# Kernel optimization log

Hardware: AMD Instinct MI355X
Metric: run time of the kernel (lower is better)

The kernel has to match this reference:

```python
import jax, jax.numpy as jnp
import numpy as np

D_MODEL = 1024
NUM_EXPERTS = 8
TOP_K = 2
B, S = 1, 2048


def setup_inputs() -> dict:
    key = jax.random.key(0)
    ks = jax.random.split(key, 8)
    sd = 1.0 / np.sqrt(D_MODEL)
    x = jax.random.normal(ks[0], (B, S, D_MODEL), dtype=jnp.float32)
    gate_w = jax.random.normal(ks[1], (D_MODEL, NUM_EXPERTS), dtype=jnp.float32) * sd
    gate_b = jnp.zeros((NUM_EXPERTS,), dtype=jnp.float32)
    w1 = jax.random.normal(ks[2], (NUM_EXPERTS, D_MODEL, 8 * D_MODEL), dtype=jnp.float32) * sd
    b1 = jnp.zeros((NUM_EXPERTS, 8 * D_MODEL), dtype=jnp.float32)
    w2 = jax.random.normal(ks[3], (NUM_EXPERTS, 4 * D_MODEL, D_MODEL), dtype=jnp.float32) * (1.0 / np.sqrt(4 * D_MODEL))
    b2 = jnp.zeros((NUM_EXPERTS, D_MODEL), dtype=jnp.float32)
    return {"x": x, "gate_w": gate_w, "gate_b": gate_b, "w1": w1, "b1": b1, "w2": w2, "b2": b2}


def reference(x, gate_w, gate_b, w1, b1, w2, b2):
    # Gating: top-k logits, softmax over the selected k
    gate_logits = jnp.einsum('bsd,de->bse', x, gate_w) + gate_b          # [B,S,E]
    weights, indices = jax.lax.top_k(gate_logits, TOP_K)                  # [B,S,K]
    weights = jax.nn.softmax(weights, axis=-1)

    # Dense all-expert compute (matches original masked-sum math; dropout in eval)
    h = jnp.einsum('bsd,edh->ebsh', x, w1) + b1[:, None, None, :]         # [E,B,S,8D]
    xh, gh = jnp.split(h, 2, axis=-1)                                     # each [E,B,S,4D]
    act = jax.nn.silu(gh) * xh
    out_e = jnp.einsum('ebsf,efd->ebsd', act, w2) + b2[:, None, None, :]  # [E,B,S,D]

    # Combine: gather the top-k expert outputs per token and weight-sum
    out_e = jnp.transpose(out_e, (1, 2, 0, 3))                            # [B,S,E,D]
    sel = jnp.take_along_axis(out_e, indices[..., None], axis=2)          # [B,S,K,D]
    return jnp.sum(sel * weights[..., None], axis=2)                      # [B,S,D]
```

## Files before the change

### kernel.cpp

```cpp
#include <hip/hip_runtime.h>
#include <hip/hip_bf16.h>

#define S 2048
#define D 1024
#define NE 8
#define HF 4096
#define HH 8192
#define BK 32
#define ACT_ROWS 4224
#define MAXRB 40
#define MAXRB2 24

typedef __attribute__((ext_vector_type(8))) __bf16 bf16x8;
typedef __attribute__((ext_vector_type(4))) float f32x4;

__device__ __forceinline__ unsigned cvtpk(float lo, float hi) {
  unsigned r;
  asm("v_cvt_pk_bf16_f32 %0, %1, %2" : "=v"(r) : "v"(lo), "v"(hi));
  return r;
}
__device__ __forceinline__ unsigned bf16b(float f) {
  unsigned b = __float_as_uint(f);
  return (b + 0x7fffu + ((b >> 16) & 1u)) >> 16;
}
__device__ __forceinline__ void gll16(const ushort* g, ushort* l) {
  __builtin_amdgcn_global_load_lds(
      (const __attribute__((address_space(1))) void*)g,
      (__attribute__((address_space(3))) void*)l, 16, 0, 0);
}

__global__ __launch_bounds__(256) void gate_kernel(
    const float* __restrict__ x, const float* __restrict__ gw,
    const float* __restrict__ gb, ushort* __restrict__ xb,
    int* __restrict__ mi0, int* __restrict__ mi1,
    float* __restrict__ mw0, float* __restrict__ mw1) {
  const int t = blockIdx.x;
  const int l = threadIdx.x;
  const float4 xv = ((const float4*)(x + (size_t)t * D))[l];
  uint2 wv = {cvtpk(xv.x, xv.y), cvtpk(xv.z, xv.w)};
  ((uint2*)(xb + (size_t)t * D))[l] = wv;

  float xa[4] = {xv.x, xv.y, xv.z, xv.w};
  float acc[NE];
#pragma unroll
  for (int e = 0; e < NE; ++e) acc[e] = 0.f;
  const float* g0 = gw + (size_t)(4 * l) * NE;
#pragma unroll
  for (int j = 0; j < 4; ++j)
#pragma unroll
    for (int e = 0; e < NE; ++e) acc[e] += xa[j] * g0[j * NE + e];
#pragma unroll
  for (int e = 0; e < NE; ++e) {
    float v = acc[e];
#pragma unroll
    for (int off = 32; off > 0; off >>= 1) v += __shfl_xor(v, off);
    acc[e] = v;
  }
  __shared__ float sm[4][NE];
  const int wid = l >> 6;
  if ((l & 63) == 0) {
#pragma unroll
    for (int e = 0; e < NE; ++e) sm[wid][e] = acc[e];
  }
  __syncthreads();
  if (l == 0) {
    float lg[NE];
#pragma unroll
    for (int e = 0; e < NE; ++e)
      lg[e] = sm[0][e] + sm[1][e] + sm[2][e] + sm[3][e] + gb[e];
    int i0 = 0; float m0 = lg[0];
#pragma unroll
    for (int e = 1; e < NE; ++e) if (lg[e] > m0) { m0 = lg[e]; i0 = e; }
    int i1 = -1; float m1 = -3.4e38f;
#pragma unroll
    for (int e = 0; e < NE; ++e) if (e != i0 && lg[e] > m1) { m1 = lg[e]; i1 = e; }
    float p = __expf(m1 - m0);
    float inv = 1.f / (1.f + p);
    mi0[t] = i0; mi1[t] = i1;
    mw0[t] = inv; mw1[t] = p * inv;
  }
}

__global__ __launch_bounds__(1024) void route_kernel(
    const int* __restrict__ mi0, const int* __restrict__ mi1,
    int* __restrict__ counts, int* __restrict__ basep, int* __restrict__ list_tok,
    int* __restrict__ mr0, int* __restrict__ mr1,
    int* __restrict__ rb_e, int* __restrict__ rb_row0, int* __restrict__ rb_n,
    int* __restrict__ rb2_e, int* __restrict__ rb2_row0, int* __restrict__ rb2_n) {
  __shared__ int cnt[NE];
  __shared__ int cur[NE];
  const int t = threadIdx.x;
  if (t < NE) cnt[t] = 0;
  __syncthreads();
  const int e0a = mi0[t], e1a = mi1[t];
  const int e0b = mi0[t + 1024], e1b = mi1[t + 1024];
  atomicAdd(&cnt[e0a], 1); atomicAdd(&cnt[e1a], 1);
  atomicAdd(&cnt[e0b], 1); atomicAdd(&cnt[e1b], 1);
  __syncthreads();
  if (t == 0) {
    int s = 0;
#pragma unroll
    for (int e = 0; e < NE; ++e) { basep[e] = s; cur[e] = s; s += cnt[e]; }
    basep[NE] = s;
    int nrb = 0, nrb2 = 0;
    for (int e = 0; e < NE; ++e) {
      for (int r0 = 0; r0 < cnt[e]; r0 += 128) {
        rb_e[nrb] = e; rb_row0[nrb] = r0; ++nrb;
      }
      for (int r0 = 0; r0 < cnt[e]; r0 += 256) {
        rb2_e[nrb2] = e; rb2_row0[nrb2] = r0; ++nrb2;
      }
    }
    *rb_n = nrb;
    *rb2_n = nrb2;
  }
  if (t < NE) counts[t] = cnt[t];
  __syncthreads();
  int r;
  r = atomicAdd(&cur[e0a], 1); list_tok[r] = t; mr0[t] = r;
  r = atomicAdd(&cur[e1a], 1); list_tok[r] = t; mr1[t] = r;
  r = atomicAdd(&cur[e0b], 1); list_tok[r] = t + 1024; mr0[t + 1024] = r;
  r = atomicAdd(&cur[e1b], 1); list_tok[r] = t + 1024; mr1[t + 1024] = r;
}

__global__ __launch_bounds__(512) void gemm1_kernel(
    const ushort* __restrict__ xb, const float* __restrict__ w1,
    const float* __restrict__ b1, const int* __restrict__ counts,
    const int* __restrict__ basep, const int* __restrict__ list_tok,
    const int* __restrict__ rb2_e, const int* __restrict__ rb2_row0,
    const int* __restrict__ rb2_n, ushort* __restrict__ act_buf) {
  const int rb = blockIdx.y;
  if (rb >= *rb2_n) return;
  const int e = rb2_e[rb];
  const int row0 = rb2_row0[rb];
  const int cnt = counts[e];
  const int jt = blockIdx.x * 64;
  const float* __restrict__ Wf = w1 + (size_t)e * D * HH;
  const int gbase = basep[e];

  __shared__ ushort As[2][256][BK];
  __shared__ unsigned Bs[2][32][68];

  const int tid = threadIdx.x;
  const int w = tid >> 6;
  const int i = tid & 63;

  const int rA0 = w * 32 + (i >> 2);
  const int rA1 = rA0 + 16;
  int s0 = row0 + rA0; if (s0 >= cnt) s0 = cnt - 1;
  int s1 = row0 + rA1; if (s1 >= cnt) s1 = cnt - 1;
  const ushort* pa0 = xb + (size_t)list_tok[gbase + s0] * D + (i & 3) * 8;
  const ushort* pa1 = xb + (size_t)list_tok[gbase + s1] * D + (i & 3) * 8;

  const int half = tid >> 8;
  const int kp = (tid >> 4) & 15;
  const int n4 = (tid & 15) * 4;
  const float* pB = Wf + (size_t)(2 * kp) * HH + jt + n4 + half * HF;

  const int wm = (w >> 1) * 64;
  const int wn = (w & 1) * 32;
  const int lr = i & 15;
  const int kg = i >> 4;

  f32x4 acc[2][4][2] = {};

  {
    float4 b0v = *(const float4*)(pB);
    float4 b1v = *(const float4*)(pB + HH);
    uint4 u = {cvtpk(b0v.x, b1v.x), cvtpk(b0v.y, b1v.y),
               cvtpk(b0v.z, b1v.z), cvtpk(b0v.w, b1v.w)};
    *(uint4*)&Bs[0][half * 16 + kp][n4] = u;
  }
  gll16(pa0, &As[0][w * 32][0]);
  gll16(pa1, &As[0][w * 32 + 16][0]);
  __syncthreads();

  int cur = 0;
#pragma unroll 1
  for (int it = 0; it < D / BK; ++it) {
    const bool pf = (it + 1 < D / BK);
    float4 b0v, b1v;
    if (pf) {
      const size_t koff = (size_t)(it + 1) * BK * HH;
      b0v = *(const float4*)(pB + koff);
      b1v = *(const float4*)(pB + koff + HH);
      const int ko = (it + 1) * BK;
      gll16(pa0 + ko, &As[cur ^ 1][w * 32][0]);
      gll16(pa1 + ko, &As[cur ^ 1][w * 32 + 16][0]);
    }
    bf16x8 af[4], bfr[2][2];
#pragma unroll
    for (int mi = 0; mi < 4; ++mi)
      af[mi] = *(const bf16x8*)&As[cur][wm + mi * 16 + lr][kg * 8];
#pragma unroll
    for (int h = 0; h < 2; ++h)
#pragma unroll
      for (int ni = 0; ni < 2; ++ni) {
        const int col = wn + ni * 16 + lr;
        uint4 tv;
        tv.x = Bs[cur][h * 16 + kg * 4 + 0][col];
        tv.y = Bs[cur][h * 16 + kg * 4 + 1][col];
        tv.z = Bs[cur][h * 16 + kg * 4 + 2][col];
        tv.w = Bs[cur][h * 16 + kg * 4 + 3][col];
        bfr[h][ni] = *(const bf16x8*)&tv;
      }
#pragma unroll
    for (int h = 0; h < 2; ++h)
#pragma unroll
      for (int mi = 0; mi < 4; ++mi)
#pragma unroll
        for (int ni = 0; ni < 2; ++ni)
          acc[h][mi][ni] = __builtin_amdgcn_mfma_f32_16x16x32_bf16(af[mi], bfr[h][ni],
                                                                   acc[h][mi][ni], 0, 0, 0);
    if (pf) {
      uint4 u = {cvtpk(b0v.x, b1v.x), cvtpk(b0v.y, b1v.y),
                 cvtpk(b0v.z, b1v.z), cvtpk(b0v.w, b1v.w)};
      *(uint4*)&Bs[cur ^ 1][half * 16 + kp][n4] = u;
    }
    __syncthreads();
    cur ^= 1;
  }

#pragma unroll
  for (int mi = 0; mi < 4; ++mi)
#pragma unroll
    for (int ni = 0; ni < 2; ++ni) {
      const int c = jt + wn + ni * 16 + lr;
      const float bx = b1[(size_t)e * HH + c];
      const float bg = b1[(size_t)e * HH + HF + c];
      f32x4 vx = acc[0][mi][ni];
      f32x4 vg = acc[1][mi][ni];
#pragma unroll
      for (int q = 0; q < 4; ++q) {
        const int slot = row0 + wm + mi * 16 + kg * 4 + q;
        if (slot < cnt) {
          float xv = vx[q] + bx;
          float g = vg[q] + bg;
          float a = g / (1.f + __expf(-g)) * xv;
          act_buf[(size_t)(gbase + slot) * HF + c] = (ushort)bf16b(a);
        }
      }
    }
}

__global__ __launch_bounds__(256) void gemm2_kernel(
    const ushort* __restrict__ act_buf, const float* __restrict__ w2,
    const int* __restrict__ counts, const int* __restrict__ basep,
    const int* __restrict__ rb_e, const int* __restrict__ rb_row0,
    const int* __restrict__ rb_n, ushort* __restrict__ oe) {
  const int rb = blockIdx.y;
  if (rb >= *rb_n) return;
  const int e = rb_e[rb];
  const int row0 = rb_row0[rb];
  const int cnt = counts[e];
  const int split = blockIdx.z;
  const int jt = blockIdx.x * 128;
  const float* __restrict__ Wf = w2 + (size_t)e * HF * D;
  const int gbase = basep[e];
  const size_t kbase = (size_t)split * (HF / 2);

  __shared__ ushort As[2][128][BK];
  __shared__ unsigned Bs[2][16][132];

  const int tid = threadIdx.x;
  const int w = tid >> 6;
  const int i = tid & 63;

  const int rA0 = w * 32 + (i >> 2);
  const ushort* pa0 = act_buf + (size_t)(gbase + row0 + rA0) * HF + kbase + (i & 3) * 8;
  const ushort* pa1 = pa0 + (size_t)16 * HF;

  const int grp = tid >> 5;
  const int n4 = (tid & 31) * 4;
  const float* pB0 = Wf + (kbase + 2 * grp) * D + jt + n4;
  const float* pB1 = pB0 + (size_t)16 * D;

  const int wm = (w >> 1) * 64;
  const int wn = (w & 1) * 64;
  const int lr = i & 15;
  const int kg = i >> 4;

  f32x4 acc[4][4] = {};

  {
    float4 a0 = *(const float4*)(pB0);
    float4 a1 = *(const float4*)(pB0 + D);
    float4 c0 = *(const float4*)(pB1);
    float4 c1 = *(const float4*)(pB1 + D);
    uint4 u0 = {cvtpk(a0.x, a1.x), cvtpk(a0.y, a1.y), cvtpk(a0.z, a1.z), cvtpk(a0.w, a1.w)};
    uint4 u1 = {cvtpk(c0.x, c1.x), cvtpk(c0.y, c1.y), cvtpk(c0.z, c1.z), cvtpk(c0.w, c1.w)};
    *(uint4*)&Bs[0][grp][n4] = u0;
    *(uint4*)&Bs[0][8 + grp][n4] = u1;
  }
  gll16(pa0, &As[0][w * 32][0]);
  gll16(pa1, &As[0][w * 32 + 16][0]);
  __syncthreads();

  int cur = 0;
#pragma unroll 1
  for (int it = 0; it < (HF / 2) / BK; ++it) {
    const bool pf = (it + 1 < (HF / 2) / BK);
    float4 a0, a1, c0, c1;
    if (pf) {
      const size_t koff = (size_t)(it + 1) * BK * D;
      a0 = *(const float4*)(pB0 + koff);
      a1 = *(const float4*)(pB0 + koff + D);
      c0 = *(const float4*)(pB1 + koff);
      c1 = *(const float4*)(pB1 + koff + D);
      const int ko = (it + 1) * BK;
      gll16(pa0 + ko, &As[cur ^ 1][w * 32][0]);
      gll16(pa1 + ko, &As[cur ^ 1][w * 32 + 16][0]);
    }
    bf16x8 af[4], bfr[4];
#pragma unroll
    for (int mi = 0; mi < 4; ++mi)
      af[mi] = *(const bf16x8*)&As[cur][wm + mi * 16 + lr][kg * 8];
#pragma unroll
    for (int ni = 0; ni < 4; ++ni) {
      const int col = wn + ni * 16 + lr;
      uint4 tv;
      tv.x = Bs[cur][kg * 4 + 0][col];
      tv.y = Bs[cur][kg * 4 + 1][col];
      tv.z = Bs[cur][kg * 4 + 2][col];
      tv.w = Bs[cur][kg * 4 + 3][col];
      bfr[ni] = *(const bf16x8*)&tv;
    }
#pragma unroll
    for (int mi = 0; mi < 4; ++mi)
#pragma unroll
      for (int ni = 0; ni < 4; ++ni)
        acc[mi][ni] = __builtin_amdgcn_mfma_f32_16x16x32_bf16(af[mi], bfr[ni],
                                                              acc[mi][ni], 0, 0, 0);
    if (pf) {
      uint4 u0 = {cvtpk(a0.x, a1.x), cvtpk(a0.y, a1.y), cvtpk(a0.z, a1.z), cvtpk(a0.w, a1.w)};
      uint4 u1 = {cvtpk(c0.x, c1.x), cvtpk(c0.y, c1.y), cvtpk(c0.z, c1.z), cvtpk(c0.w, c1.w)};
      *(uint4*)&Bs[cur ^ 1][grp][n4] = u0;
      *(uint4*)&Bs[cur ^ 1][8 + grp][n4] = u1;
    }
    __syncthreads();
    cur ^= 1;
  }

#pragma unroll
  for (int mi = 0; mi < 4; ++mi)
#pragma unroll
    for (int ni = 0; ni < 4; ++ni) {
      f32x4 v = acc[mi][ni];
#pragma unroll
      for (int q = 0; q < 4; ++q) {
        const int slot = row0 + wm + mi * 16 + kg * 4 + q;
        if (slot < cnt)
          oe[((size_t)split * ACT_ROWS + gbase + slot) * D + jt + wn + ni * 16 + lr] =
              (ushort)bf16b(v[q]);
      }
    }
}

__global__ void combine_kernel(const ushort* __restrict__ oe,
                               const int* __restrict__ mr0, const int* __restrict__ mr1,
                               const float* __restrict__ mw0, const float* __restrict__ mw1,
                               const int* __restrict__ mi0, const int* __restrict__ mi1,
                               const float* __restrict__ b2, float* __restrict__ out) {
  const int t = blockIdx.x;
  const int l = threadIdx.x;
  const float w0 = mw0[t], w1 = mw1[t];
  const int r0 = mr0[t], r1 = mr1[t];
  float a0[4] = {0.f, 0.f, 0.f, 0.f}, a1[4] = {0.f, 0.f, 0.f, 0.f};
#pragma unroll
  for (int s = 0; s < 2; ++s) {
    uint2 u0 = *(const uint2*)(oe + ((size_t)s * ACT_ROWS + r0) * D + l * 4);
    uint2 u1 = *(const uint2*)(oe + ((size_t)s * ACT_ROWS + r1) * D + l * 4);
    a0[0] += __uint_as_float(u0.x << 16);
    a0[1] += __uint_as_float(u0.x & 0xffff0000u);
    a0[2] += __uint_as_float(u0.y << 16);
    a0[3] += __uint_as_float(u0.y & 0xffff0000u);
    a1[0] += __uint_as_float(u1.x << 16);
    a1[1] += __uint_as_float(u1.x & 0xffff0000u);
    a1[2] += __uint_as_float(u1.y << 16);
    a1[3] += __uint_as_float(u1.y & 0xffff0000u);
  }
  float4 c0 = ((const float4*)(b2 + (size_t)mi0[t] * D))[l];
  float4 c1 = ((const float4*)(b2 + (size_t)mi1[t] * D))[l];
  float4 r;
  r.x = w0 * (a0[0] + c0.x) + w1 * (a1[0] + c1.x);
  r.y = w0 * (a0[1] + c0.y) + w1 * (a1[1] + c1.y);
  r.z = w0 * (a0[2] + c0.z) + w1 * (a1[2] + c1.z);
  r.w = w0 * (a0[3] + c0.w) + w1 * (a1[3] + c1.w);
  ((float4*)(out + (size_t)t * D))[l] = r;
}

extern "C" void kernel_launch(void* const* d_in, const int* in_sizes, int n_in,
                              void* d_out, int out_size, void* d_ws, size_t ws_size,
                              hipStream_t stream) {
  const float* x  = (const float*)d_in[0];
  const float* gw = (const float*)d_in[1];
  const float* gb = (const float*)d_in[2];
  const float* w1 = (const float*)d_in[3];
  const float* b1 = (const float*)d_in[4];
  const float* w2 = (const float*)d_in[5];
  const float* b2 = (const float*)d_in[6];
  float* out = (float*)d_out;

  char* ws = (char*)d_ws;
  int*   counts   = (int*)(ws + 0);
  int*   basep    = (int*)(ws + 64);
  int*   rb_n     = (int*)(ws + 128);
  int*   rb_e     = (int*)(ws + 192);
  int*   rb_row0  = (int*)(ws + 384);
  int*   rb2_n    = (int*)(ws + 576);
  int*   rb2_e    = (int*)(ws + 640);
  int*   rb2_row0 = (int*)(ws + 768);
  int*   mi0      = (int*)(ws + 1024);
  int*   mi1      = (int*)(ws + 1024 + 1 * 8192);
  int*   mr0      = (int*)(ws + 1024 + 2 * 8192);
  int*   mr1      = (int*)(ws + 1024 + 3 * 8192);
  float* mw0      = (float*)(ws + 1024 + 4 * 8192);
  float* mw1      = (float*)(ws + 1024 + 5 * 8192);
  int*   list_tok = (int*)(ws + 1024 + 6 * 8192);
  ushort* xb      = (ushort*)(ws + 66560);
  ushort* act_buf = (ushort*)(ws + 4260864);
  ushort* oe      = (ushort*)(ws + 38863872);

  gate_kernel<<<S, 256, 0, stream>>>(x, gw, gb, xb, mi0, mi1, mw0, mw1);
  route_kernel<<<1, 1024, 0, stream>>>(mi0, mi1, counts, basep, list_tok, mr0, mr1,
                                       rb_e, rb_row0, rb_n, rb2_e, rb2_row0, rb2_n);
  gemm1_kernel<<<dim3(64, MAXRB2), 512, 0, stream>>>(xb, w1, b1, counts, basep, list_tok,
                                                     rb2_e, rb2_row0, rb2_n, act_buf);
  gemm2_kernel<<<dim3(8, MAXRB, 2), 256, 0, stream>>>(act_buf, w2, counts, basep,
                                                      rb_e, rb_row0, rb_n, oe);
  combine_kernel<<<S, 256, 0, stream>>>(oe, mr0, mr1, mw0, mw1, mi0, mi1, b2, out);
}
```

Measured before the change: 261.4 us.

## Load A fragments directly from global into registers, bypassing LDS staging

Both expert GEMM kernels stop staging the activation (A) tile through shared memory via global_load_lds. Each lane now loads its own MFMA A fragment straight from global memory into registers, double-buffered in registers with a 2x manually unrolled loop. This removes the A-tile LDS traffic and its share of the LDS footprint. In exchange, each A row is fetched redundantly by every wave that uses it (two waves in gemm1 and gemm2), uncoalesced gather loads sit on the critical path, and register pressure rises.

```diff
diff --git a/kernel.cpp b/kernel.cpp
--- a/kernel.cpp
+++ b/kernel.cpp
@@ -22,11 +22,6 @@
 __device__ __forceinline__ unsigned bf16b(float f) {
   unsigned b = __float_as_uint(f);
   return (b + 0x7fffu + ((b >> 16) & 1u)) >> 16;
-}
-__device__ __forceinline__ void gll16(const ushort* g, ushort* l) {
-  __builtin_amdgcn_global_load_lds(
-      (const __attribute__((address_space(1))) void*)g,
-      (__attribute__((address_space(3))) void*)l, 16, 0, 0);
 }
 
 __global__ __launch_bounds__(256) void gate_kernel(
@@ -122,6 +117,47 @@
   r = atomicAdd(&cur[e0b], 1); list_tok[r] = t + 1024; mr0[t + 1024] = r;
   r = atomicAdd(&cur[e1b], 1); list_tok[r] = t + 1024; mr1[t + 1024] = r;
 }
+
+#define G1_STEP(AFUSE, AFLOAD, IT, CUR)                                        \
+  {                                                                            \
+    const bool pf = ((IT) + 1 < D / BK);                                       \
+    float4 b0v, b1v;                                                           \
+    if (pf) {                                                                  \
+      const size_t koff = (size_t)((IT) + 1) * BK;                             \
+      b0v = *(const float4*)(pB + koff * HH);                                  \
+      b1v = *(const float4*)(pB + koff * HH + HH);                             \
+      _Pragma("unroll")                                                        \
+      for (int mi = 0; mi < 4; ++mi)                                           \
+        AFLOAD[mi] = *(const uint4*)(pA[mi] + koff);                           \
+    }                                                                          \
+    bf16x8 bfr[2][2];                                                          \
+    _Pragma("unroll")                                                          \
+    for (int h = 0; h < 2; ++h)                                                \
+      _Pragma("unroll")                                                        \
+      for (int ni = 0; ni < 2; ++ni) {                                         \
+        const int col = wn + ni * 16 + lr;                                     \
+        uint4 tv;                                                              \
+        tv.x = Bs[CUR][h * 16 + kg * 4 + 0][col];                              \
+        tv.y = Bs[CUR][h * 16 + kg * 4 + 1][col];                              \
+        tv.z = Bs[CUR][h * 16 + kg * 4 + 2][col];                              \
+        tv.w = Bs[CUR][h * 16 + kg * 4 + 3][col];                              \
+        bfr[h][ni] = *(const bf16x8*)&tv;                                      \
+      }                                                                        \
+    _Pragma("unroll")                                                          \
+    for (int h = 0; h < 2; ++h)                                                \
+      _Pragma("unroll")                                                        \
+      for (int mi = 0; mi < 4; ++mi)                                           \
+        _Pragma("unroll")                                                      \
+        for (int ni = 0; ni < 2; ++ni)                                         \
+          acc[h][mi][ni] = __builtin_amdgcn_mfma_f32_16x16x32_bf16(            \
+              *(const bf16x8*)&AFUSE[mi], bfr[h][ni], acc[h][mi][ni], 0, 0, 0);\
+    if (pf) {                                                                  \
+      uint4 u = {cvtpk(b0v.x, b1v.x), cvtpk(b0v.y, b1v.y),                     \
+                 cvtpk(b0v.z, b1v.z), cvtpk(b0v.w, b1v.w)};                    \
+      *(uint4*)&Bs[(CUR) ^ 1][half * 16 + kp][n4] = u;                         \
+    }                                                                          \
+    __syncthreads();                                                           \
+  }
 
 __global__ __launch_bounds__(512) void gemm1_kernel(
     const ushort* __restrict__ xb, const float* __restrict__ w1,
@@ -138,31 +174,31 @@
   const float* __restrict__ Wf = w1 + (size_t)e * D * HH;
   const int gbase = basep[e];
 
-  __shared__ ushort As[2][256][BK];
   __shared__ unsigned Bs[2][32][68];
 
   const int tid = threadIdx.x;
   const int w = tid >> 6;
   const int i = tid & 63;
-
-  const int rA0 = w * 32 + (i >> 2);
-  const int rA1 = rA0 + 16;
-  int s0 = row0 + rA0; if (s0 >= cnt) s0 = cnt - 1;
-  int s1 = row0 + rA1; if (s1 >= cnt) s1 = cnt - 1;
-  const ushort* pa0 = xb + (size_t)list_tok[gbase + s0] * D + (i & 3) * 8;
-  const ushort* pa1 = xb + (size_t)list_tok[gbase + s1] * D + (i & 3) * 8;
+  const int lr = i & 15;
+  const int kg = i >> 4;
+  const int wm = (w >> 1) * 64;
+  const int wn = (w & 1) * 32;
+
+  const ushort* pA[4];
+#pragma unroll
+  for (int mi = 0; mi < 4; ++mi) {
+    int rr = row0 + wm + mi * 16 + lr;
+    int ss = (rr < cnt) ? rr : cnt - 1;
+    pA[mi] = xb + (size_t)list_tok[gbase + ss] * D + kg * 8;
+  }
 
   const int half = tid >> 8;
   const int kp = (tid >> 4) & 15;
   const int n4 = (tid & 15) * 4;
   const float* pB = Wf + (size_t)(2 * kp) * HH + jt + n4 + half * HF;
 
-  const int wm = (w >> 1) * 64;
-  const int wn = (w & 1) * 32;
-  const int lr = i & 15;
-  const int kg = i >> 4;
-
   f32x4 acc[2][4][2] = {};
+  uint4 afA[4], afB[4];
 
   {
     float4 b0v = *(const float4*)(pB);
@@ -171,54 +207,14 @@
                cvtpk(b0v.z, b1v.z), cvtpk(b0v.w, b1v.w)};
     *(uint4*)&Bs[0][half * 16 + kp][n4] = u;
   }
-  gll16(pa0, &As[0][w * 32][0]);
-  gll16(pa1, &As[0][w * 32 + 16][0]);
-  __syncthreads();
-
-  int cur = 0;
+#pragma unroll
+  for (int mi = 0; mi < 4; ++mi) afA[mi] = *(const uint4*)(pA[mi]);
+  __syncthreads();
+
 #pragma unroll 1
-  for (int it = 0; it < D / BK; ++it) {
-    const bool pf = (it + 1 < D / BK);
-    float4 b0v, b1v;
-    if (pf) {
-      const size_t koff = (size_t)(it + 1) * BK * HH;
-      b0v = *(const float4*)(pB + koff);
-      b1v = *(const float4*)(pB + koff + HH);
-      const int ko = (it + 1) * BK;
-      gll16(pa0 + ko, &As[cur ^ 1][w * 32][0]);
-      gll16(pa1 + ko, &As[cur ^ 1][w * 32 + 16][0]);
-    }
-    bf16x8 af[4], bfr[2][2];
-#pragma unroll
-    for (int mi = 0; mi < 4; ++mi)
-      af[mi] = *(const bf16x8*)&As[cur][wm + mi * 16 + lr][kg * 8];
-#pragma unroll
-    for (int h = 0; h < 2; ++h)
-#pragma unroll
-      for (int ni = 0; ni < 2; ++ni) {
-        const int col = wn + ni * 16 + lr;
-        uint4 tv;
-        tv.x = Bs[cur][h * 16 + kg * 4 + 0][col];
-        tv.y = Bs[cur][h * 16 + kg * 4 + 1][col];
-        tv.z = Bs[cur][h * 16 + kg * 4 + 2][col];
-        tv.w = Bs[cur][h * 16 + kg * 4 + 3][col];
-        bfr[h][ni] = *(const bf16x8*)&tv;
-      }
-#pragma unroll
-    for (int h = 0; h < 2; ++h)
-#pragma unroll
-      for (int mi = 0; mi < 4; ++mi)
-#pragma unroll
-        for (int ni = 0; ni < 2; ++ni)
-          acc[h][mi][ni] = __builtin_amdgcn_mfma_f32_16x16x32_bf16(af[mi], bfr[h][ni],
-                                                                   acc[h][mi][ni], 0, 0, 0);
-    if (pf) {
-      uint4 u = {cvtpk(b0v.x, b1v.x), cvtpk(b0v.y, b1v.y),
-                 cvtpk(b0v.z, b1v.z), cvtpk(b0v.w, b1v.w)};
-      *(uint4*)&Bs[cur ^ 1][half * 16 + kp][n4] = u;
-    }
-    __syncthreads();
-    cur ^= 1;
+  for (int it = 0; it < D / BK; it += 2) {
+    G1_STEP(afA, afB, it, 0);
+    G1_STEP(afB, afA, it + 1, 1);
   }
 
 #pragma unroll
@@ -242,6 +238,48 @@
       }
     }
 }
+
+#define G2_STEP(AFUSE, AFLOAD, IT, CUR)                                        \
+  {                                                                            \
+    const bool pf = ((IT) + 1 < (HF / 2) / BK);                                \
+    float4 a0, a1, c0, c1;                                                     \
+    if (pf) {                                                                  \
+      const size_t koff = (size_t)((IT) + 1) * BK;                             \
+      a0 = *(const float4*)(pB0 + koff * D);                                   \
+      a1 = *(const float4*)(pB0 + koff * D + D);                               \
+      c0 = *(const float4*)(pB1 + koff * D);                                   \
+      c1 = *(const float4*)(pB1 + koff * D + D);                               \
+      _Pragma("unroll")                                                        \
+      for (int mi = 0; mi < 4; ++mi)                                           \
+        AFLOAD[mi] = *(const uint4*)(pA[mi] + koff);                           \
+    }                                                                          \
+    bf16x8 bfr[4];                                                             \
+    _Pragma("unroll")                                                          \
+    for (int ni = 0; ni < 4; ++ni) {                                           \
+      const int col = wn + ni * 16 + lr;                                       \
+      uint4 tv;                                                                \
+      tv.x = Bs[CUR][kg * 4 + 0][col];                                         \
+      tv.y = Bs[CUR][kg * 4 + 1][col];                                         \
+      tv.z = Bs[CUR][kg * 4 + 2][col];                                         \
+      tv.w = Bs[CUR][kg * 4 + 3][col];                                         \
+      bfr[ni] = *(const bf16x8*)&tv;                                           \
+    }                                                                          \
+    _Pragma("unroll")                                                          \
+    for (int mi = 0; mi < 4; ++mi)                                             \
+      _Pragma("unroll")                                                        \
+      for (int ni = 0; ni < 4; ++ni)                                           \
+        acc[mi][ni] = __builtin_amdgcn_mfma_f32_16x16x32_bf16(                 \
+            *(const bf16x8*)&AFUSE[mi], bfr[ni], acc[mi][ni], 0, 0, 0);        \
+    if (pf) {                                                                  \
+      uint4 u0 = {cvtpk(a0.x, a1.x), cvtpk(a0.y, a1.y),                        \
+                  cvtpk(a0.z, a1.z), cvtpk(a0.w, a1.w)};                       \
+      uint4 u1 = {cvtpk(c0.x, c1.x), cvtpk(c0.y, c1.y),                        \
+                  cvtpk(c0.z, c1.z), cvtpk(c0.w, c1.w)};                       \
+      *(uint4*)&Bs[(CUR) ^ 1][grp][n4] = u0;                                   \
+      *(uint4*)&Bs[(CUR) ^ 1][8 + grp][n4] = u1;                               \
+    }                                                                          \
+    __syncthreads();                                                           \
+  }
 
 __global__ __launch_bounds__(256) void gemm2_kernel(
     const ushort* __restrict__ act_buf, const float* __restrict__ w2,
@@ -259,28 +297,28 @@
   const int gbase = basep[e];
   const size_t kbase = (size_t)split * (HF / 2);
 
-  __shared__ ushort As[2][128][BK];
   __shared__ unsigned Bs[2][16][132];
 
   const int tid = threadIdx.x;
   const int w = tid >> 6;
   const int i = tid & 63;
-
-  const int rA0 = w * 32 + (i >> 2);
-  const ushort* pa0 = act_buf + (size_t)(gbase + row0 + rA0) * HF + kbase + (i & 3) * 8;
-  const ushort* pa1 = pa0 + (size_t)16 * HF;
+  const int lr = i & 15;
+  const int kg = i >> 4;
+  const int wm = (w >> 1) * 64;
+  const int wn = (w & 1) * 64;
+
+  const ushort* pA[4];
+#pragma unroll
+  for (int mi = 0; mi < 4; ++mi)
+    pA[mi] = act_buf + (size_t)(gbase + row0 + wm + mi * 16 + lr) * HF + kbase + kg * 8;
 
   const int grp = tid >> 5;
   const int n4 = (tid & 31) * 4;
   const float* pB0 = Wf + (kbase + 2 * grp) * D + jt + n4;
   const float* pB1 = pB0 + (size_t)16 * D;
 
-  const int wm = (w >> 1) * 64;
-  const int wn = (w & 1) * 64;
-  const int lr = i & 15;
-  const int kg = i >> 4;
-
   f32x4 acc[4][4] = {};
+  uint4 afA[4], afB[4];
 
   {
     float4 a0 = *(const float4*)(pB0);
@@ -292,53 +330,14 @@
     *(uint4*)&Bs[0][grp][n4] = u0;
     *(uint4*)&Bs[0][8 + grp][n4] = u1;
   }
-  gll16(pa0, &As[0][w * 32][0]);
-  gll16(pa1, &As[0][w * 32 + 16][0]);
-  __syncthreads();
-
-  int cur = 0;
+#pragma unroll
+  for (int mi = 0; mi < 4; ++mi) afA[mi] = *(const uint4*)(pA[mi]);
+  __syncthreads();
+
 #pragma unroll 1
-  for (int it = 0; it < (HF / 2) / BK; ++it) {
-    const bool pf = (it + 1 < (HF / 2) / BK);
-    float4 a0, a1, c0, c1;
-    if (pf) {
-      const size_t koff = (size_t)(it + 1) * BK * D;
-      a0 = *(const float4*)(pB0 + koff);
-      a1 = *(const float4*)(pB0 + koff + D);
-      c0 = *(const float4*)(pB1 + koff);
-      c1 = *(const float4*)(pB1 + koff + D);
-      const int ko = (it + 1) * BK;
-      gll16(pa0 + ko, &As[cur ^ 1][w * 32][0]);
-      gll16(pa1 + ko, &As[cur ^ 1][w * 32 + 16][0]);
-    }
-    bf16x8 af[4], bfr[4];
-#pragma unroll
-    for (int mi = 0; mi < 4; ++mi)
-      af[mi] = *(const bf16x8*)&As[cur][wm + mi * 16 + lr][kg * 8];
-#pragma unroll
-    for (int ni = 0; ni < 4; ++ni) {
-      const int col = wn + ni * 16 + lr;
-      uint4 tv;
-      tv.x = Bs[cur][kg * 4 + 0][col];
-      tv.y = Bs[cur][kg * 4 + 1][col];
-      tv.z = Bs[cur][kg * 4 + 2][col];
-      tv.w = Bs[cur][kg * 4 + 3][col];
-      bfr[ni] = *(const bf16x8*)&tv;
-    }
-#pragma unroll
-    for (int mi = 0; mi < 4; ++mi)
-#pragma unroll
-      for (int ni = 0; ni < 4; ++ni)
-        acc[mi][ni] = __builtin_amdgcn_mfma_f32_16x16x32_bf16(af[mi], bfr[ni],
-                                                              acc[mi][ni], 0, 0, 0);
-    if (pf) {
-      uint4 u0 = {cvtpk(a0.x, a1.x), cvtpk(a0.y, a1.y), cvtpk(a0.z, a1.z), cvtpk(a0.w, a1.w)};
-      uint4 u1 = {cvtpk(c0.x, c1.x), cvtpk(c0.y, c1.y), cvtpk(c0.z, c1.z), cvtpk(c0.w, c1.w)};
-      *(uint4*)&Bs[cur ^ 1][grp][n4] = u0;
-      *(uint4*)&Bs[cur ^ 1][8 + grp][n4] = u1;
-    }
-    __syncthreads();
-    cur ^= 1;
+  for (int it = 0; it < (HF / 2) / BK; it += 2) {
+    G2_STEP(afA, afB, it, 0);
+    G2_STEP(afB, afA, it + 1, 1);
   }
 
 #pragma unroll
```

Result: slower. 430.7 us (+64.8%).
